# Optimization experiments

Hardware: AMD Instinct MI355X
Metric: run time of the kernel (lower is better)

## Reference

```python
import jax, jax.numpy as jnp
import numpy as np

BATCH, TIME, IN_DIM = 32, 512, 256
LSTM_DIM, PROJ_DIM, OUT_DIM = 1024, 512, 256


def setup_inputs() -> dict:
    key = jax.random.key(0)
    ks = jax.random.split(key, 8)
    s = 1.0 / np.sqrt(LSTM_DIM)
    u = lambda k, shape: (2.0 * jax.random.uniform(k, shape) - 1.0) * s
    return {
        "inputs": jax.random.normal(ks[0], (BATCH, TIME, IN_DIM), dtype=jnp.float32),
        "W": u(ks[1], (IN_DIM, 4 * LSTM_DIM)),
        "R": u(ks[2], (PROJ_DIM, 4 * LSTM_DIM)),
        "W_proj": u(ks[3], (LSTM_DIM, PROJ_DIM)),
        "p": u(ks[4], (3 * LSTM_DIM,)),
        "b": u(ks[5], (4 * LSTM_DIM,)),
        "lin_w": u(ks[6], (OUT_DIM, PROJ_DIM)),
        "lin_b": u(ks[7], (OUT_DIM,)),
    }


def _lstmp(inputs, W, R, W_proj, p, b):
    B, T, _ = inputs.shape
    H = p.shape[0] // 3
    P = W_proj.shape[1]
    pi, pf, po = p[:H], p[H:2 * H], p[2 * H:]
    # precompute input contribution to all gates: [T, B, 4H]
    xg = jnp.einsum('bti,ig->tbg', inputs, W) + b

    def step(carry, xg_t):
        hp, c = carry  # [B,P], [B,H]
        z = xg_t + hp @ R  # [B, 4H]
        i = jax.nn.sigmoid(z[:, :H] + c * pi)
        f = jax.nn.sigmoid(z[:, H:2 * H] + c * pf)
        g = jnp.tanh(z[:, 2 * H:3 * H])
        c_new = f * c + i * g
        o = jax.nn.sigmoid(z[:, 3 * H:] + c_new * po)
        h = o * jnp.tanh(c_new)
        hp_new = h @ W_proj
        return (hp_new, c_new), hp_new

    hp0 = jnp.zeros((B, P), dtype=inputs.dtype)
    c0 = jnp.zeros((B, H), dtype=inputs.dtype)
    _, hp_seq = jax.lax.scan(step, (hp0, c0), xg)  # [T, B, P]
    return jnp.transpose(hp_seq, (1, 0, 2))  # [B, T, P]


def reference(inputs, W, R, W_proj, p, b, lin_w, lin_b):
    hp = _lstmp(inputs, W, R, W_proj, p, b)
    return hp @ lin_w.T + lin_b
```

## Files before the change

### kernel.cpp

```cpp
#include <hip/hip_runtime.h>
#include <math.h>

#define B_SZ   32
#define T_SZ   512
#define I_DIM  256
#define H_DIM  1024
#define P_DIM  512
#define G4     4096
#define O_DIM  256

typedef short short8 __attribute__((ext_vector_type(8)));
typedef float f32x4  __attribute__((ext_vector_type(4)));

__device__ __forceinline__ float sigmf(float x) { return 1.0f / (1.0f + __expf(-x)); }
__device__ __forceinline__ float tanhfast(float x) { return 1.0f - 2.0f / (__expf(2.0f * x) + 1.0f); }
__device__ __forceinline__ short f2bf(float f) {
    union { float f; unsigned u; } v; v.f = f;
    unsigned r = (v.u + 0x7FFF + ((v.u >> 16) & 1)) >> 16;
    return (short)r;
}
__device__ __forceinline__ float bf2f(short h) {
    union { unsigned u; float f; } v; v.u = ((unsigned)(unsigned short)h) << 16;
    return v.f;
}

__global__ void split_copy(const float* __restrict__ in, short* __restrict__ hi,
                           short* __restrict__ lo, int n)
{
    int i = blockIdx.x * 256 + threadIdx.x;
    if (i < n) {
        float v = in[i];
        short h = f2bf(v);
        hi[i] = h;
        if (lo) lo[i] = f2bf(v - bf2f(h));
    }
}

__global__ void transpose_split(const float* __restrict__ in, short* __restrict__ hi,
                                short* __restrict__ lo, int rows, int cols)
{
    __shared__ float t[32][33];
    int c0 = blockIdx.x * 32, r0 = blockIdx.y * 32;
    int x = threadIdx.x, y = threadIdx.y;
    #pragma unroll
    for (int i = y; i < 32; i += 8) t[i][x] = in[(size_t)(r0 + i) * cols + c0 + x];
    __syncthreads();
    #pragma unroll
    for (int i = y; i < 32; i += 8) {
        float v = t[x][i];
        short h = f2bf(v);
        size_t o = (size_t)(c0 + i) * rows + r0 + x;
        hi[o] = h;
        if (lo) lo[o] = f2bf(v - bf2f(h));
    }
}

template<int SPLIT, int AMODE, int CMODE, int BIAS>
__device__ __forceinline__
void gemm_tile(const short* __restrict__ Ah, const short* __restrict__ Al,
               const short* __restrict__ Bh, const short* __restrict__ Bl,
               const float* __restrict__ bias, void* __restrict__ Cp,
               int N, int K, int t0, int m0, int n0)
{
    __shared__ short As[SPLIT + 1][8192];
    __shared__ short Bs[SPLIT + 1][8192];
    const int tid = threadIdx.x;
    const int l   = tid & 63;
    const int w   = tid >> 6;
    const int wm  = w & 1, wn = w >> 1;

    f32x4 acc[4][4] = {};

    for (int k0 = 0; k0 < K; k0 += 64) {
        __syncthreads();
        #pragma unroll
        for (int q = 0; q < 4; q++) {
            int rg   = q * 4 + w;
            int rr   = (rg << 3) + (l >> 3);
            int slot = (l & 7) ^ (rr & 7);
            int lidx = rg * 512 + l * 8;
            size_t aoff, boff;
            int ra = m0 + rr, rb = n0 + rr;
            if constexpr (AMODE == 1)
                aoff = (size_t)((ra & 31) * 512 + t0 + (ra >> 5)) * 256 + k0 + slot * 8;
            else
                aoff = (size_t)ra * K + k0 + slot * 8;
            boff = (size_t)rb * K + k0 + slot * 8;
            __builtin_amdgcn_global_load_lds(Ah + aoff, &As[0][lidx], 16, 0, 0);
            __builtin_amdgcn_global_load_lds(Bh + boff, &Bs[0][lidx], 16, 0, 0);
            if constexpr (SPLIT) {
                __builtin_amdgcn_global_load_lds(Al + aoff, &As[1][lidx], 16, 0, 0);
                __builtin_amdgcn_global_load_lds(Bl + boff, &Bs[1][lidx], 16, 0, 0);
            }
        }
        __syncthreads();

        #pragma unroll
        for (int ks = 0; ks < 2; ks++) {
            const int cb = (((ks * 4) + (l >> 4)) ^ (l & 7)) * 16;
            short8 af[4], bfr[4], afl[4], bfl[4];
            #pragma unroll
            for (int mf = 0; mf < 4; mf++) {
                int mloc = wm * 64 + mf * 16 + (l & 15);
                af[mf] = *(const short8*)((const char*)As[0] + mloc * 128 + cb);
                if constexpr (SPLIT)
                    afl[mf] = *(const short8*)((const char*)As[1] + mloc * 128 + cb);
            }
            #pragma unroll
            for (int nf = 0; nf < 4; nf++) {
                int nloc = wn * 64 + nf * 16 + (l & 15);
                bfr[nf] = *(const short8*)((const char*)Bs[0] + nloc * 128 + cb);
                if constexpr (SPLIT)
                    bfl[nf] = *(const short8*)((const char*)Bs[1] + nloc * 128 + cb);
            }
            #pragma unroll
            for (int mf = 0; mf < 4; mf++)
                #pragma unroll
                for (int nf = 0; nf < 4; nf++)
                    acc[mf][nf] = __builtin_amdgcn_mfma_f32_16x16x32_bf16(
                        af[mf], bfr[nf], acc[mf][nf], 0, 0, 0);
            if constexpr (SPLIT) {
                #pragma unroll
                for (int mf = 0; mf < 4; mf++)
                    #pragma unroll
                    for (int nf = 0; nf < 4; nf++)
                        acc[mf][nf] = __builtin_amdgcn_mfma_f32_16x16x32_bf16(
                            af[mf], bfl[nf], acc[mf][nf], 0, 0, 0);
                #pragma unroll
                for (int mf = 0; mf < 4; mf++)
                    #pragma unroll
                    for (int nf = 0; nf < 4; nf++)
                        acc[mf][nf] = __builtin_amdgcn_mfma_f32_16x16x32_bf16(
                            afl[mf], bfr[nf], acc[mf][nf], 0, 0, 0);
            }
        }
    }

    float bv[4];
    if constexpr (BIAS) {
        #pragma unroll
        for (int nf = 0; nf < 4; nf++)
            bv[nf] = bias[n0 + wn * 64 + nf * 16 + (l & 15)];
    }
    #pragma unroll
    for (int mf = 0; mf < 4; mf++) {
        #pragma unroll
        for (int r = 0; r < 4; r++) {
            int row = m0 + wm * 64 + mf * 16 + (l >> 4) * 4 + r;
            #pragma unroll
            for (int nf = 0; nf < 4; nf++) {
                int col = n0 + wn * 64 + nf * 16 + (l & 15);
                float v = acc[mf][nf][r];
                if constexpr (BIAS) v += bv[nf];
                if constexpr (CMODE == 0)
                    ((float*)Cp)[(size_t)row * N + col] = v;
                else if constexpr (CMODE == 1)
                    ((short*)Cp)[(size_t)row * N + col] = f2bf(v);
                else
                    ((float*)Cp)[(size_t)(row & 31) * (T_SZ * O_DIM)
                                 + (size_t)(row >> 5) * O_DIM + col] = v;
            }
        }
    }
}

__global__ __launch_bounds__(256)
void gemm_rr(const short* Ah, const short* Al, const short* Bh, const short* Bl,
             const float* bias, void* Cp, int N, int K, int t0)
{ gemm_tile<1, 0, 0, 0>(Ah, Al, Bh, Bl, bias, Cp, N, K, t0, blockIdx.y * 128, blockIdx.x * 128); }

__global__ __launch_bounds__(256)
void gemm_xg(const short* Ah, const short* Al, const short* Bh, const short* Bl,
             const float* bias, void* Cp, int N, int K, int t0)
{ gemm_tile<0, 1, 0, 1>(Ah, Al, Bh, Bl, bias, Cp, N, K, t0, blockIdx.y * 128, blockIdx.x * 128); }

__global__ __launch_bounds__(256)
void gemm_proj(const short* Ah, const short* Al, const short* Bh, const short* Bl,
               const float* bias, void* Cp, int N, int K, int t0)
{ gemm_tile<0, 0, 1, 0>(Ah, Al, Bh, Bl, bias, Cp, N, K, t0, blockIdx.y * 128, blockIdx.x * 128); }

__global__ __launch_bounds__(256)
void gemm_out(const short* Ah, const short* Al, const short* Bh, const short* Bl,
              const float* bias, void* Cp, int N, int K, int t0)
{ gemm_tile<0, 0, 2, 1>(Ah, Al, Bh, Bl, bias, Cp, N, K, t0, blockIdx.y * 128, blockIdx.x * 128); }

__global__ __launch_bounds__(256)
void pack_rr(const float* __restrict__ RRf, short* __restrict__ RRbp)
{
    int idx = blockIdx.x * 256 + threadIdx.x;
    int lane = idx & 63;
    int kt   = (idx >> 6) & 31;
    int blk  = idx >> 11;
    int nl = lane & 15;
    int g = nl >> 2, jl = nl & 3;
    int col = g * 1024 + blk * 4 + jl;
    int kbase = kt * 32 + (lane >> 4) * 8;
    short8 v;
    #pragma unroll
    for (int i = 0; i < 8; i++)
        v[i] = f2bf(RRf[(size_t)(kbase + i) * G4 + col]);
    ((short8*)RRbp)[idx] = v;
}

__global__ __launch_bounds__(256)
void lstm_step(const float* __restrict__ xg_t,
               const short* __restrict__ RRbp,
               const short* __restrict__ hp_in,
               short* __restrict__ hp_out,
               short* __restrict__ h_bf_t,
               float* __restrict__ c_st,
               const float* __restrict__ p)
{
    __shared__ float zbuf[2][32][17];
    const int tid  = threadIdx.x;
    const int bid  = blockIdx.x;
    const int lane = tid & 63;
    const int w    = tid >> 6;
    const int wm   = w & 1;
    const int kh   = w >> 1;

    const int eb = tid >> 2, ejl = tid & 3;
    const int ej = bid * 4 + ejl;
    float xzi = 0.f, xzf = 0.f, xzg = 0.f, xzo = 0.f, cv = 0.f;
    if (tid < 128) {
        const float* xr = xg_t + (size_t)eb * G4 + ej;
        xzi = xr[0]; xzf = xr[1024]; xzg = xr[2048]; xzo = xr[3072];
        cv = c_st[eb * H_DIM + ej];
    }

    const short8* Ap = (const short8*)hp_in + (size_t)(wm * 32 + kh * 16) * 64 + lane;
    const short8* Bp = (const short8*)RRbp + (size_t)(bid * 32 + kh * 16) * 64 + lane;

    f32x4 acc0 = {0.f, 0.f, 0.f, 0.f};
    f32x4 acc1 = {0.f, 0.f, 0.f, 0.f};
    #pragma unroll
    for (int i = 0; i < 8; i++) {
        short8 a = Ap[(size_t)i * 64];
        short8 b = Bp[(size_t)i * 64];
        acc0 = __builtin_amdgcn_mfma_f32_16x16x32_bf16(a, b, acc0, 0, 0, 0);
    }
    #pragma unroll
    for (int i = 8; i < 16; i++) {
        short8 a = Ap[(size_t)i * 64];
        short8 b = Bp[(size_t)i * 64];
        acc1 = __builtin_amdgcn_mfma_f32_16x16x32_bf16(a, b, acc1, 0, 0, 0);
    }
    acc0[0] += acc1[0]; acc0[1] += acc1[1]; acc0[2] += acc1[2]; acc0[3] += acc1[3];

    {
        int col = lane & 15;
        int row = (lane >> 4) * 4;
        #pragma unroll
        for (int r = 0; r < 4; r++)
            zbuf[kh][wm * 16 + row + r][col] = acc0[r];
    }
    __syncthreads();

    if (tid < 128) {
        float zi = zbuf[0][eb][ejl]      + zbuf[1][eb][ejl]      + xzi;
        float zf = zbuf[0][eb][4 + ejl]  + zbuf[1][eb][4 + ejl]  + xzf;
        float zg = zbuf[0][eb][8 + ejl]  + zbuf[1][eb][8 + ejl]  + xzg;
        float zo = zbuf[0][eb][12 + ejl] + zbuf[1][eb][12 + ejl] + xzo;
        float ig = sigmf(zi + cv * p[ej]);
        float fg = sigmf(zf + cv * p[1024 + ej]);
        float gg = tanhfast(zg);
        float cn = fg * cv + ig * gg;
        float og = sigmf(zo + cn * p[2048 + ej]);
        float hv = og * tanhfast(cn);
        short hb = f2bf(hv);
        c_st[eb * H_DIM + ej]   = cn;
        h_bf_t[eb * H_DIM + ej] = hb;
        int lane2 = (eb & 15) | (((ej & 31) >> 3) << 4);
        int kt2   = ej >> 5;
        int wm2   = eb >> 4;
        hp_out[(size_t)(((wm2 * 32 + kt2) * 64 + lane2)) * 8 + (ej & 7)] = hb;
    }
}

extern "C" void kernel_launch(void* const* d_in, const int* in_sizes, int n_in,
                              void* d_out, int out_size, void* d_ws, size_t ws_size,
                              hipStream_t stream)
{
    const float* inp    = (const float*)d_in[0];
    const float* W      = (const float*)d_in[1];
    const float* R      = (const float*)d_in[2];
    const float* W_proj = (const float*)d_in[3];
    const float* p      = (const float*)d_in[4];
    const float* bvec   = (const float*)d_in[5];
    const float* lin_w  = (const float*)d_in[6];
    const float* lin_b  = (const float*)d_in[7];
    float* out = (float*)d_out;
    char* ws = (char*)d_ws;

    float* RRbuf = (float*)(ws + 0);
    short* RRbp  = (short*)(ws + 16777216);
    short* Wp_hi = (short*)(ws + 25165824);
    short* Wp_lo = (short*)(ws + 26214400);
    short* Rt_hi = (short*)(ws + 27262976);
    short* Rt_lo = (short*)(ws + 31457280);
    short* Wt_hi = (short*)(ws + 35651584);
    short* in_hi = (short*)(ws + 39845888);
    short* Wpt   = (short*)(ws + 56623104);
    short* lwb   = (short*)(ws + 57671680);
    float* c_st  = (float*)(ws + 57933824);
    short* hpk0  = (short*)(ws + 58064896);
    short* hpk1  = (short*)(ws + 58130432);
    short* h_bf  = (short*)(ws + 58195968);
    float* xg_c  = (float*)(ws + 91750400);
    short* hp_bf = (short*)(ws + 125304832);

    hipMemsetAsync(hpk0, 0, 65536, stream);
    hipMemsetAsync(c_st, 0, B_SZ * H_DIM * sizeof(float), stream);

    split_copy<<<(H_DIM * P_DIM + 255) / 256, 256, 0, stream>>>(W_proj, Wp_hi, Wp_lo, H_DIM * P_DIM);
    split_copy<<<(B_SZ * T_SZ * I_DIM + 255) / 256, 256, 0, stream>>>(inp, in_hi, nullptr, B_SZ * T_SZ * I_DIM);
    split_copy<<<(O_DIM * P_DIM + 255) / 256, 256, 0, stream>>>(lin_w, lwb, nullptr, O_DIM * P_DIM);
    transpose_split<<<dim3(G4 / 32, P_DIM / 32), dim3(32, 8), 0, stream>>>(R, Rt_hi, Rt_lo, P_DIM, G4);
    transpose_split<<<dim3(G4 / 32, I_DIM / 32), dim3(32, 8), 0, stream>>>(W, Wt_hi, nullptr, I_DIM, G4);
    transpose_split<<<dim3(P_DIM / 32, H_DIM / 32), dim3(32, 8), 0, stream>>>(W_proj, Wpt, nullptr, H_DIM, P_DIM);

    gemm_rr<<<dim3(G4 / 128, H_DIM / 128), 256, 0, stream>>>(
        Wp_hi, Wp_lo, Rt_hi, Rt_lo, nullptr, RRbuf, G4, P_DIM, 0);
    pack_rr<<<2048, 256, 0, stream>>>(RRbuf, RRbp);

    for (int chunk = 0; chunk < 8; chunk++) {
        int t0 = chunk * 64;
        gemm_xg<<<dim3(G4 / 128, 2048 / 128), 256, 0, stream>>>(
            in_hi, nullptr, Wt_hi, nullptr, bvec, xg_c, G4, I_DIM, t0);
        for (int tl = 0; tl < 64; tl++) {
            int t = t0 + tl;
            short* hin  = (t & 1) ? hpk1 : hpk0;
            short* hout = (t & 1) ? hpk0 : hpk1;
            lstm_step<<<256, 256, 0, stream>>>(
                xg_c + (size_t)tl * B_SZ * G4, RRbp, hin, hout,
                h_bf + (size_t)t * (B_SZ * H_DIM), c_st, p);
        }
    }

    gemm_proj<<<dim3(P_DIM / 128, 16384 / 128), 256, 0, stream>>>(
        h_bf, nullptr, Wpt, nullptr, nullptr, hp_bf, P_DIM, H_DIM, 0);

    gemm_out<<<dim3(O_DIM / 128, 16384 / 128), 256, 0, stream>>>(
        hp_bf, nullptr, lwb, nullptr, lin_b, out, O_DIM, P_DIM, 0);
}
```

Before: 2.364 ms.

## Fuse input projection into LSTM step and fold W_proj into output linear

The chunked xg GEMM and its fp32 gate buffer are removed. Each recurrent step now does the x_t·W product with extra MFMAs on pre-packed bf16 inputs and weights, and adds the bias inside the step. The separate projection GEMM is also removed by precomputing W_proj·lin_wᵀ (a split-precision 1024x256 product), so the output GEMM reads h directly with K=1024. This cuts kernel launches and the large xg write/read traffic. In exchange, every serial step does more work, and the reassociation changes rounding, since h is used in bf16 against a combined weight.

```diff
diff --git a/kernel.cpp b/kernel.cpp
--- a/kernel.cpp
+++ b/kernel.cpp
@@ -170,16 +170,6 @@
 { gemm_tile<1, 0, 0, 0>(Ah, Al, Bh, Bl, bias, Cp, N, K, t0, blockIdx.y * 128, blockIdx.x * 128); }
 
 __global__ __launch_bounds__(256)
-void gemm_xg(const short* Ah, const short* Al, const short* Bh, const short* Bl,
-             const float* bias, void* Cp, int N, int K, int t0)
-{ gemm_tile<0, 1, 0, 1>(Ah, Al, Bh, Bl, bias, Cp, N, K, t0, blockIdx.y * 128, blockIdx.x * 128); }
-
-__global__ __launch_bounds__(256)
-void gemm_proj(const short* Ah, const short* Al, const short* Bh, const short* Bl,
-               const float* bias, void* Cp, int N, int K, int t0)
-{ gemm_tile<0, 0, 1, 0>(Ah, Al, Bh, Bl, bias, Cp, N, K, t0, blockIdx.y * 128, blockIdx.x * 128); }
-
-__global__ __launch_bounds__(256)
 void gemm_out(const short* Ah, const short* Al, const short* Bh, const short* Bl,
               const float* bias, void* Cp, int N, int K, int t0)
 { gemm_tile<0, 0, 2, 1>(Ah, Al, Bh, Bl, bias, Cp, N, K, t0, blockIdx.y * 128, blockIdx.x * 128); }
@@ -203,13 +193,50 @@
 }
 
 __global__ __launch_bounds__(256)
-void lstm_step(const float* __restrict__ xg_t,
+void pack_w(const float* __restrict__ Wf, short* __restrict__ Wbp)
+{
+    int idx = blockIdx.x * 256 + threadIdx.x;
+    int lane = idx & 63;
+    int kt   = (idx >> 6) & 7;
+    int blk  = idx >> 9;
+    int nl = lane & 15;
+    int g = nl >> 2, jl = nl & 3;
+    int col = g * 1024 + blk * 4 + jl;
+    int kbase = kt * 32 + (lane >> 4) * 8;
+    short8 v;
+    #pragma unroll
+    for (int i = 0; i < 8; i++)
+        v[i] = f2bf(Wf[(size_t)(kbase + i) * G4 + col]);
+    ((short8*)Wbp)[idx] = v;
+}
+
+__global__ __launch_bounds__(256)
+void pack_x(const float* __restrict__ inp, short* __restrict__ xpk)
+{
+    int idx = blockIdx.x * 256 + threadIdx.x;
+    int lane = idx & 63;
+    int kt   = (idx >> 6) & 7;
+    int wm   = (idx >> 9) & 1;
+    int t    = idx >> 10;
+    int b = wm * 16 + (lane & 15);
+    int kbase = kt * 32 + (lane >> 4) * 8;
+    const float* src = inp + ((size_t)b * T_SZ + t) * I_DIM + kbase;
+    short8 v;
+    #pragma unroll
+    for (int i = 0; i < 8; i++) v[i] = f2bf(src[i]);
+    ((short8*)xpk)[idx] = v;
+}
+
+__global__ __launch_bounds__(256)
+void lstm_step(const short* __restrict__ xpk_t,
+               const short* __restrict__ Wbp,
                const short* __restrict__ RRbp,
                const short* __restrict__ hp_in,
                short* __restrict__ hp_out,
                short* __restrict__ h_bf_t,
                float* __restrict__ c_st,
-               const float* __restrict__ p)
+               const float* __restrict__ p,
+               const float* __restrict__ bvec)
 {
     __shared__ float zbuf[2][32][17];
     const int tid  = threadIdx.x;
@@ -221,18 +248,32 @@
 
     const int eb = tid >> 2, ejl = tid & 3;
     const int ej = bid * 4 + ejl;
-    float xzi = 0.f, xzf = 0.f, xzg = 0.f, xzo = 0.f, cv = 0.f;
+    float bzi = 0.f, bzf = 0.f, bzg = 0.f, bzo = 0.f, cv = 0.f;
     if (tid < 128) {
-        const float* xr = xg_t + (size_t)eb * G4 + ej;
-        xzi = xr[0]; xzf = xr[1024]; xzg = xr[2048]; xzo = xr[3072];
+        bzi = bvec[ej]; bzf = bvec[1024 + ej];
+        bzg = bvec[2048 + ej]; bzo = bvec[3072 + ej];
         cv = c_st[eb * H_DIM + ej];
     }
 
-    const short8* Ap = (const short8*)hp_in + (size_t)(wm * 32 + kh * 16) * 64 + lane;
-    const short8* Bp = (const short8*)RRbp + (size_t)(bid * 32 + kh * 16) * 64 + lane;
+    const short8* Ap  = (const short8*)hp_in + (size_t)(wm * 32 + kh * 16) * 64 + lane;
+    const short8* Bp  = (const short8*)RRbp + (size_t)(bid * 32 + kh * 16) * 64 + lane;
+    const short8* Apx = (const short8*)xpk_t + (size_t)(wm * 8 + kh * 4) * 64 + lane;
+    const short8* Bpx = (const short8*)Wbp + (size_t)(bid * 8 + kh * 4) * 64 + lane;
 
     f32x4 acc0 = {0.f, 0.f, 0.f, 0.f};
     f32x4 acc1 = {0.f, 0.f, 0.f, 0.f};
+    #pragma unroll
+    for (int i = 0; i < 2; i++) {
+        short8 a = Apx[(size_t)i * 64];
+        short8 b = Bpx[(size_t)i * 64];
+        acc0 = __builtin_amdgcn_mfma_f32_16x16x32_bf16(a, b, acc0, 0, 0, 0);
+    }
+    #pragma unroll
+    for (int i = 2; i < 4; i++) {
+        short8 a = Apx[(size_t)i * 64];
+        short8 b = Bpx[(size_t)i * 64];
+        acc1 = __builtin_amdgcn_mfma_f32_16x16x32_bf16(a, b, acc1, 0, 0, 0);
+    }
     #pragma unroll
     for (int i = 0; i < 8; i++) {
         short8 a = Ap[(size_t)i * 64];
@@ -257,10 +298,10 @@
     __syncthreads();
 
     if (tid < 128) {
-        float zi = zbuf[0][eb][ejl]      + zbuf[1][eb][ejl]      + xzi;
-        float zf = zbuf[0][eb][4 + ejl]  + zbuf[1][eb][4 + ejl]  + xzf;
-        float zg = zbuf[0][eb][8 + ejl]  + zbuf[1][eb][8 + ejl]  + xzg;
-        float zo = zbuf[0][eb][12 + ejl] + zbuf[1][eb][12 + ejl] + xzo;
+        float zi = zbuf[0][eb][ejl]      + zbuf[1][eb][ejl]      + bzi;
+        float zf = zbuf[0][eb][4 + ejl]  + zbuf[1][eb][4 + ejl]  + bzf;
+        float zg = zbuf[0][eb][8 + ejl]  + zbuf[1][eb][8 + ejl]  + bzg;
+        float zo = zbuf[0][eb][12 + ejl] + zbuf[1][eb][12 + ejl] + bzo;
         float ig = sigmf(zi + cv * p[ej]);
         float fg = sigmf(zf + cv * p[1024 + ej]);
         float gg = tanhfast(zg);
@@ -298,48 +339,43 @@
     short* Wp_lo = (short*)(ws + 26214400);
     short* Rt_hi = (short*)(ws + 27262976);
     short* Rt_lo = (short*)(ws + 31457280);
-    short* Wt_hi = (short*)(ws + 35651584);
-    short* in_hi = (short*)(ws + 39845888);
-    short* Wpt   = (short*)(ws + 56623104);
-    short* lwb   = (short*)(ws + 57671680);
-    float* c_st  = (float*)(ws + 57933824);
-    short* hpk0  = (short*)(ws + 58064896);
-    short* hpk1  = (short*)(ws + 58130432);
-    short* h_bf  = (short*)(ws + 58195968);
-    float* xg_c  = (float*)(ws + 91750400);
-    short* hp_bf = (short*)(ws + 125304832);
+    short* lwb_h = (short*)(ws + 35651584);
+    short* lwb_l = (short*)(ws + 35913728);
+    short* Wbp   = (short*)(ws + 36175872);
+    short* xpk   = (short*)(ws + 38273024);
+    float* PLbuf = (float*)(ws + 46661632);
+    short* PLt   = (short*)(ws + 47710208);
+    float* c_st  = (float*)(ws + 48234496);
+    short* hpk0  = (short*)(ws + 48365568);
+    short* hpk1  = (short*)(ws + 48431104);
+    short* h_bf  = (short*)(ws + 48496640);
 
     hipMemsetAsync(hpk0, 0, 65536, stream);
     hipMemsetAsync(c_st, 0, B_SZ * H_DIM * sizeof(float), stream);
 
+    pack_x<<<2048, 256, 0, stream>>>(inp, xpk);
+    pack_w<<<512, 256, 0, stream>>>(W, Wbp);
     split_copy<<<(H_DIM * P_DIM + 255) / 256, 256, 0, stream>>>(W_proj, Wp_hi, Wp_lo, H_DIM * P_DIM);
-    split_copy<<<(B_SZ * T_SZ * I_DIM + 255) / 256, 256, 0, stream>>>(inp, in_hi, nullptr, B_SZ * T_SZ * I_DIM);
-    split_copy<<<(O_DIM * P_DIM + 255) / 256, 256, 0, stream>>>(lin_w, lwb, nullptr, O_DIM * P_DIM);
+    split_copy<<<(O_DIM * P_DIM + 255) / 256, 256, 0, stream>>>(lin_w, lwb_h, lwb_l, O_DIM * P_DIM);
     transpose_split<<<dim3(G4 / 32, P_DIM / 32), dim3(32, 8), 0, stream>>>(R, Rt_hi, Rt_lo, P_DIM, G4);
-    transpose_split<<<dim3(G4 / 32, I_DIM / 32), dim3(32, 8), 0, stream>>>(W, Wt_hi, nullptr, I_DIM, G4);
-    transpose_split<<<dim3(P_DIM / 32, H_DIM / 32), dim3(32, 8), 0, stream>>>(W_proj, Wpt, nullptr, H_DIM, P_DIM);
 
     gemm_rr<<<dim3(G4 / 128, H_DIM / 128), 256, 0, stream>>>(
         Wp_hi, Wp_lo, Rt_hi, Rt_lo, nullptr, RRbuf, G4, P_DIM, 0);
     pack_rr<<<2048, 256, 0, stream>>>(RRbuf, RRbp);
 
-    for (int chunk = 0; chunk < 8; chunk++) {
-        int t0 = chunk * 64;
-        gemm_xg<<<dim3(G4 / 128, 2048 / 128), 256, 0, stream>>>(
-            in_hi, nullptr, Wt_hi, nullptr, bvec, xg_c, G4, I_DIM, t0);
-        for (int tl = 0; tl < 64; tl++) {
-            int t = t0 + tl;
-            short* hin  = (t & 1) ? hpk1 : hpk0;
-            short* hout = (t & 1) ? hpk0 : hpk1;
-            lstm_step<<<256, 256, 0, stream>>>(
-                xg_c + (size_t)tl * B_SZ * G4, RRbp, hin, hout,
-                h_bf + (size_t)t * (B_SZ * H_DIM), c_st, p);
-        }
-    }
-
-    gemm_proj<<<dim3(P_DIM / 128, 16384 / 128), 256, 0, stream>>>(
-        h_bf, nullptr, Wpt, nullptr, nullptr, hp_bf, P_DIM, H_DIM, 0);
+    gemm_rr<<<dim3(O_DIM / 128, H_DIM / 128), 256, 0, stream>>>(
+        Wp_hi, Wp_lo, lwb_h, lwb_l, nullptr, PLbuf, O_DIM, P_DIM, 0);
+    transpose_split<<<dim3(O_DIM / 32, H_DIM / 32), dim3(32, 8), 0, stream>>>(
+        PLbuf, PLt, nullptr, H_DIM, O_DIM);
+
+    for (int t = 0; t < T_SZ; t++) {
+        short* hin  = (t & 1) ? hpk1 : hpk0;
+        short* hout = (t & 1) ? hpk0 : hpk1;
+        lstm_step<<<256, 256, 0, stream>>>(
+            xpk + (size_t)t * (2 * 8 * 64 * 8), Wbp, RRbp, hin, hout,
+            h_bf + (size_t)t * (B_SZ * H_DIM), c_st, p, bvec);
+    }
 
     gemm_out<<<dim3(O_DIM / 128, 16384 / 128), 256, 0, stream>>>(
-        hp_bf, nullptr, lwb, nullptr, lin_b, out, O_DIM, P_DIM, 0);
-}
+        h_bf, nullptr, PLt, nullptr, lin_b, out, O_DIM, H_DIM, 0);
+}
```

Result: faster. 2.147 ms (-9.2%).
